# Kernel tuning notes

Hardware: AMD Instinct MI355X
Metric: run time of the kernel (lower is better)

The kernel has to match this reference:

```python
import jax, jax.numpy as jnp
import numpy as np

NS = 100000   # served nodes
NI = 100000   # interfered nodes
E = 1000000   # edges per relation
D = 64        # 2 * Nt_num, Nt_num = 32
HM = 32       # message MLP hidden
HU = 16       # update MLP hidden


def _lin_init(key, fan_in, fan_out):
    s = 1.0 / np.sqrt(fan_in)
    kw, kb = jax.random.split(key)
    w = jax.random.uniform(kw, (fan_in, fan_out), jnp.float32, -s, s)
    b = jax.random.uniform(kb, (fan_out,), jnp.float32, -s, s)
    return w, b


def setup_inputs() -> dict:
    key = jax.random.key(0)
    ks = jax.random.split(key, 12)
    wm1, bm1 = _lin_init(ks[0], D, HM)
    wm2, bm2 = _lin_init(ks[1], HM, D)
    wu1, bu1 = _lin_init(ks[2], D, HU)
    wu2, bu2 = _lin_init(ks[3], HU, D)
    wo, bo = _lin_init(ks[4], D, D)
    edge_s2i = jnp.stack([
        jax.random.randint(ks[5], (E,), 0, NS),   # src in served
        jax.random.randint(ks[6], (E,), 0, NI),   # dst in interfered
    ]).astype(jnp.int64)
    edge_i2s = jnp.stack([
        jax.random.randint(ks[7], (E,), 0, NI),   # src in interfered
        jax.random.randint(ks[8], (E,), 0, NS),   # dst in served
    ]).astype(jnp.int64)
    return {
        "x_served": jax.random.normal(ks[9], (NS, D), jnp.float32),
        "x_interfered": jax.random.normal(ks[10], (NI, D), jnp.float32),
        "edge_s2i": edge_s2i,
        "edge_i2s": edge_i2s,
        "wm1": wm1, "bm1": bm1, "wm2": wm2, "bm2": bm2,
        "wu1": wu1, "bu1": bu1, "wu2": wu2, "bu2": bu2,
        "wo": wo, "bo": bo,
    }


def reference(x_served, x_interfered, edge_s2i, edge_i2s,
              wm1, bm1, wm2, bm2, wu1, bu1, wu2, bu2, wo, bo):
    def mlp_m(h):  # MLP([D, 32, D]): Lin+ReLU, Lin+ReLU
        return jax.nn.relu(jax.nn.relu(h @ wm1 + bm1) @ wm2 + bm2)

    def mlp_u(h):  # MLP([D, 16, D])
        return jax.nn.relu(jax.nn.relu(h @ wu1 + bu1) @ wu2 + bu2)

    def conv(x_src, edges, n_dst):
        # gather source node features per edge, per-edge message MLP
        msg = mlp_m(x_src[edges[0]])                    # [E, D]
        # scatter-sum into destination nodes
        agg = jax.ops.segment_sum(msg, edges[1], num_segments=n_dst)
        return mlp_u(agg)                               # [n_dst, D]

    xs, xi = x_served, x_interfered
    for _ in range(3):
        new_i = conv(xs, edge_s2i, NI)   # served -> interfered
        new_s = conv(xi, edge_i2s, NS)   # interfered -> served
        xs, xi = new_s, new_i
    # h2o on served: Lin + Tanh -> beamforming matrix
    return jnp.tanh(xs @ wo + bo)
```

## Files before the change

kernel.cpp:

```cpp
#include <hip/hip_runtime.h>
#include <hip/hip_fp16.h>
#include <math.h>

constexpr int D = 64;
constexpr int CAP = 48;
constexpr int RPB = 256;
constexpr int EPB = 4096;

typedef _Float16 half2_t __attribute__((ext_vector_type(2)));
typedef _Float16 f16x8 __attribute__((ext_vector_type(8)));
typedef float f32x4 __attribute__((ext_vector_type(4)));

__device__ inline float fdot2(unsigned a, unsigned b, float c){
    return __builtin_amdgcn_fdot2(__builtin_bit_cast(half2_t, a),
                                  __builtin_bit_cast(half2_t, b), c, false);
}

__device__ inline unsigned pack2(float lo, float hi){
    __half2 h = __floats2half2_rn(lo, hi);
    return *(unsigned*)&h;
}

__device__ inline void ld16u(const unsigned* base, unsigned* w){
    const uint4* p = (const uint4*)base;
    uint4 a = p[0], b = p[1], c = p[2], d = p[3];
    w[0]=a.x;  w[1]=a.y;  w[2]=a.z;  w[3]=a.w;
    w[4]=b.x;  w[5]=b.y;  w[6]=b.z;  w[7]=b.w;
    w[8]=c.x;  w[9]=c.y;  w[10]=c.z; w[11]=c.w;
    w[12]=d.x; w[13]=d.y; w[14]=d.z; w[15]=d.w;
}

__device__ inline void store_half8(__half* dst, const float* o){
    uint4 w;
    w.x = pack2(o[0], o[1]); w.y = pack2(o[2], o[3]);
    w.z = pack2(o[4], o[5]); w.w = pack2(o[6], o[7]);
    *((uint4*)dst) = w;
}

__device__ inline void load_half8(const __half* src, float* r){
    uint4 w = *((const uint4*)src);
    __half2* h = (__half2*)&w;
    float2 f0 = __half22float2(h[0]);
    float2 f1 = __half22float2(h[1]);
    float2 f2 = __half22float2(h[2]);
    float2 f3 = __half22float2(h[3]);
    r[0] = f0.x; r[1] = f0.y; r[2] = f1.x; r[3] = f1.y;
    r[4] = f2.x; r[5] = f2.y; r[6] = f3.x; r[7] = f3.y;
}


__global__ void __launch_bounds__(256) k_bucket_mlpm(
        const int* __restrict__ es2i, const int* __restrict__ ei2s, int E, int NI,
        int NBUK, int BSTRIDE,
        int* __restrict__ gcur, unsigned* __restrict__ buckets,
        const float* __restrict__ x,
        const float* __restrict__ wm1, const float* __restrict__ bm1,
        const float* __restrict__ wm2, const float* __restrict__ bm2,
        __half* __restrict__ y, int Nmlp, int nbEdge)
{
    __shared__ __align__(16) char smem[8704];
    int t = threadIdx.x;

    if ((int)blockIdx.x < nbEdge){
        int* hist = (int*)smem;
        int* base = (int*)(smem + 4096);
        for (int i = t; i < NBUK; i += 256) hist[i] = 0;
        __syncthreads();
        int e0 = blockIdx.x * EPB + t;
        int rr[16], ss[16];
        #pragma unroll
        for (int k = 0; k < 16; k++){
            int i = e0 + k*256;
            if (i < E){
                ss[k] = es2i[i];            rr[k] = es2i[E + i];
            } else if (i < 2*E){
                int j = i - E;
                ss[k] = ei2s[j];            rr[k] = NI + ei2s[E + j];
            } else rr[k] = -1;
        }
        #pragma unroll
        for (int k = 0; k < 16; k++)
            if (rr[k] >= 0) atomicAdd(&hist[rr[k] >> 8], 1);
        __syncthreads();
        for (int b = t; b < NBUK; b += 256){
            int h = hist[b];
            base[b] = h ? atomicAdd(&gcur[b], h) : 0;
        }
        __syncthreads();
        #pragma unroll
        for (int k = 0; k < 16; k++){
            if (rr[k] >= 0){
                int b = rr[k] >> 8;
                int p = atomicAdd(&base[b], 1);
                if (p < BSTRIDE)
                    buckets[(size_t)b*BSTRIDE + p] =
                        ((unsigned)(rr[k] & 255) << 24) | (unsigned)ss[k];
            }
        }
        return;
    }

    unsigned* w1p = (unsigned*)smem;
    unsigned* w2p = (unsigned*)(smem + 4096);
    float*    sb1 = (float*)(smem + 8192);
    float*    sb2 = (float*)(smem + 8320);
    for (int i = t; i < 1024; i += 256){ int kp=i>>5, j=i&31; w1p[i]=pack2(wm1[(2*kp)*32+j], wm1[(2*kp+1)*32+j]); }
    for (int i = t; i < 1024; i += 256){ int jp=i>>6, c=i&63; w2p[i]=pack2(wm2[(2*jp)*64+c], wm2[(2*jp+1)*64+c]); }
    if (t < 32) sb1[t] = bm1[t];
    if (t < 64) sb2[t] = bm2[t];
    __syncthreads();
    int n = ((int)blockIdx.x - nbEdge)*256 + t;
    if (n >= Nmlp) return;

    const float4* xp = (const float4*)(x + (size_t)n*D);
    unsigned xq[32];
    #pragma unroll
    for (int i = 0; i < 16; i++){
        float4 v = xp[i];
        xq[2*i]   = pack2(v.x, v.y);
        xq[2*i+1] = pack2(v.z, v.w);
    }
    float h[32];
    #pragma unroll
    for (int j = 0; j < 32; j++) h[j] = 0.f;
    #pragma unroll
    for (int kp = 0; kp < 32; kp++){
        unsigned xv = xq[kp];
        unsigned w[32];
        ld16u(&w1p[kp*32],      w);
        ld16u(&w1p[kp*32 + 16], w + 16);
        #pragma unroll
        for (int j = 0; j < 32; j++) h[j] = fdot2(xv, w[j], h[j]);
    }
    #pragma unroll
    for (int j = 0; j < 32; j++) h[j] = fmaxf(h[j] + sb1[j], 0.f);
    unsigned hh[16];
    #pragma unroll
    for (int jp = 0; jp < 16; jp++) hh[jp] = pack2(h[2*jp], h[2*jp+1]);

    __half* yrow = y + (size_t)n*D;
    #pragma unroll
    for (int c0 = 0; c0 < 64; c0 += 32){
        float o[32];
        #pragma unroll
        for (int c = 0; c < 32; c++) o[c] = sb2[c0 + c];
        #pragma unroll
        for (int jp = 0; jp < 16; jp++){
            unsigned hv = hh[jp];
            unsigned w[32];
            ld16u(&w2p[jp*64 + c0],      w);
            ld16u(&w2p[jp*64 + c0 + 16], w + 16);
            #pragma unroll
            for (int c = 0; c < 32; c++) o[c] = fdot2(hv, w[c], o[c]);
        }
        #pragma unroll
        for (int c = 0; c < 32; c++) o[c] = fmaxf(o[c], 0.f);
        store_half8(yrow + c0,      &o[0]);
        store_half8(yrow + c0 + 8,  &o[8]);
        store_half8(yrow + c0 + 16, &o[16]);
        store_half8(yrow + c0 + 24, &o[24]);
    }
}


__global__ void __launch_bounds__(512) k_scatter_lds(const int* __restrict__ gcur,
        const unsigned* __restrict__ buckets, int BSTRIDE, int NTOT,
        int* __restrict__ cnt, int* __restrict__ slots)
{
    __shared__ int lcnt[RPB];
    __shared__ int lslots[RPB*CAP];
    int t = threadIdx.x;
    int b = blockIdx.x;
    int r0 = b * RPB;
    int nrows = NTOT - r0; if (nrows > RPB) nrows = RPB;

    for (int i = t; i < RPB; i += 512) lcnt[i] = 0;
    __syncthreads();

    int n = gcur[b]; if (n > BSTRIDE) n = BSTRIDE;
    const unsigned* bp = buckets + (size_t)b*BSTRIDE;
    for (int k = t; k < n; k += 512){
        unsigned e = bp[k];
        int lr  = e >> 24;
        int src = e & 0xFFFFFF;
        int pos = atomicAdd(&lcnt[lr], 1);
        if (pos < CAP) lslots[lr*CAP + pos] = src;
    }
    __syncthreads();

    int4* gs = (int4*)(slots + (size_t)r0*CAP);
    const int4* ls = (const int4*)lslots;
    int n4 = nrows*CAP/4;
    for (int i = t; i < n4; i += 512) gs[i] = ls[i];
    for (int i = t; i < nrows; i += 512) cnt[r0 + i] = lcnt[i];
}


__global__ void __launch_bounds__(256) k_agg(const __half* __restrict__ M,
        const int* __restrict__ cnt, const int* __restrict__ slots,
        __half* __restrict__ agg, int N)
{
    int gid  = blockIdx.x*256 + threadIdx.x;
    int node = gid >> 6;
    if (node >= N) return;
    int lane = gid & 63;
    int sub  = lane >> 3;
    int fl   = lane & 7;
    int deg = cnt[node]; deg = deg < CAP ? deg : CAP;
    const int* row = slots + (size_t)node*CAP;
    float acc[8];
    #pragma unroll
    for (int i = 0; i < 8; i++) acc[i] = 0.f;
    for (int k = sub; k < deg; k += 8){
        int s = row[k];
        float v[8];
        load_half8(M + (size_t)s*D + fl*8, v);
        #pragma unroll
        for (int i = 0; i < 8; i++) acc[i] += v[i];
    }
    #pragma unroll
    for (int i = 0; i < 8; i++){
        acc[i] += __shfl_xor(acc[i], 8);
        acc[i] += __shfl_xor(acc[i], 16);
        acc[i] += __shfl_xor(acc[i], 32);
    }
    if (sub == 0) store_half8(agg + (size_t)node*D + fl*8, acc);
}


__global__ void __launch_bounds__(256) k_mlp_um(const __half* __restrict__ agg,
        const float* __restrict__ wu1, const float* __restrict__ bu1,
        const float* __restrict__ wu2, const float* __restrict__ bu2,
        const float* __restrict__ wm1, const float* __restrict__ bm1,
        const float* __restrict__ wm2, const float* __restrict__ bm2,
        __half* __restrict__ y, int N)
{
    __shared__ float  lds_h [4][16][20];
    __shared__ float  lds_y [4][16][68];
    __shared__ float  lds_hm[4][16][36];
    __shared__ __half lds_m [4][16][72];

    int t  = threadIdx.x;
    int wv = t >> 6, l = t & 63;
    int m  = l & 15, g = l >> 4;

    f16x8 Bu1[2], Bu2[4], Bm1[2][2], Bm2[4];
    #pragma unroll
    for (int kt = 0; kt < 2; kt++)
        #pragma unroll
        for (int i = 0; i < 8; i++)
            Bu1[kt][i] = (_Float16)wu1[(kt*32 + 8*g + i)*16 + m];
    #pragma unroll
    for (int jb = 0; jb < 4; jb++)
        #pragma unroll
        for (int i = 0; i < 8; i++){
            int k = 8*g + i;
            Bu2[jb][i] = (k < 16) ? (_Float16)wu2[k*64 + jb*16 + m] : (_Float16)0.f;
        }
    #pragma unroll
    for (int kt = 0; kt < 2; kt++)
        #pragma unroll
        for (int nt = 0; nt < 2; nt++)
            #pragma unroll
            for (int i = 0; i < 8; i++)
                Bm1[kt][nt][i] = (_Float16)wm1[(kt*32 + 8*g + i)*32 + nt*16 + m];
    #pragma unroll
    for (int jb = 0; jb < 4; jb++)
        #pragma unroll
        for (int i = 0; i < 8; i++)
            Bm2[jb][i] = (_Float16)wm2[(8*g + i)*64 + jb*16 + m];

    float bu1v = bu1[m];
    float bu2v[4], bm2v[4], bm1v[2];
    #pragma unroll
    for (int jb = 0; jb < 4; jb++){ bu2v[jb] = bu2[jb*16 + m]; bm2v[jb] = bm2[jb*16 + m]; }
    #pragma unroll
    for (int nt = 0; nt < 2; nt++) bm1v[nt] = bm1[nt*16 + m];

    #pragma unroll
    for (int tile = 0; tile < 2; tile++){
        int nb = blockIdx.x*128 + tile*64 + wv*16;
        if (nb >= N) break;

        int an = nb + m; if (an >= N) an = N - 1;
        const __half* arow = agg + (size_t)an*64;
        f16x8 Ax0 = *reinterpret_cast<const f16x8*>(arow + 8*g);
        f16x8 Ax1 = *reinterpret_cast<const f16x8*>(arow + 32 + 8*g);

        f32x4 acc = {0.f, 0.f, 0.f, 0.f};
        acc = __builtin_amdgcn_mfma_f32_16x16x32_f16(Ax0, Bu1[0], acc, 0, 0, 0);
        acc = __builtin_amdgcn_mfma_f32_16x16x32_f16(Ax1, Bu1[1], acc, 0, 0, 0);
        #pragma unroll
        for (int r = 0; r < 4; r++)
            lds_h[wv][4*g + r][m] = fmaxf(acc[r] + bu1v, 0.f);

        f16x8 Ah;
        #pragma unroll
        for (int i = 0; i < 8; i++){
            int k = 8*g + i;
            Ah[i] = (k < 16) ? (_Float16)lds_h[wv][m][k] : (_Float16)0.f;
        }

        #pragma unroll
        for (int jb = 0; jb < 4; jb++){
            f32x4 a2 = {0.f, 0.f, 0.f, 0.f};
            a2 = __builtin_amdgcn_mfma_f32_16x16x32_f16(Ah, Bu2[jb], a2, 0, 0, 0);
            #pragma unroll
            for (int r = 0; r < 4; r++)
                lds_y[wv][4*g + r][jb*16 + m] = fmaxf(a2[r] + bu2v[jb], 0.f);
        }

        f16x8 Ay0, Ay1;
        #pragma unroll
        for (int i = 0; i < 8; i++){
            Ay0[i] = (_Float16)lds_y[wv][m][8*g + i];
            Ay1[i] = (_Float16)lds_y[wv][m][32 + 8*g + i];
        }

        #pragma unroll
        for (int nt = 0; nt < 2; nt++){
            f32x4 a3 = {0.f, 0.f, 0.f, 0.f};
            a3 = __builtin_amdgcn_mfma_f32_16x16x32_f16(Ay0, Bm1[0][nt], a3, 0, 0, 0);
            a3 = __builtin_amdgcn_mfma_f32_16x16x32_f16(Ay1, Bm1[1][nt], a3, 0, 0, 0);
            #pragma unroll
            for (int r = 0; r < 4; r++)
                lds_hm[wv][4*g + r][nt*16 + m] = fmaxf(a3[r] + bm1v[nt], 0.f);
        }

        f16x8 Ahm;
        #pragma unroll
        for (int i = 0; i < 8; i++)
            Ahm[i] = (_Float16)lds_hm[wv][m][8*g + i];

        #pragma unroll
        for (int jb = 0; jb < 4; jb++){
            f32x4 a4 = {0.f, 0.f, 0.f, 0.f};
            a4 = __builtin_amdgcn_mfma_f32_16x16x32_f16(Ahm, Bm2[jb], a4, 0, 0, 0);
            #pragma unroll
            for (int r = 0; r < 4; r++)
                lds_m[wv][4*g + r][jb*16 + m] = __float2half(fmaxf(a4[r] + bm2v[jb], 0.f));
        }

        int lr = l >> 2;
        int node = nb + lr;
        if (node < N){
            uint4* dst = (uint4*)(y + (size_t)node*64);
            const uint4* src = (const uint4*)&lds_m[wv][lr][0];
            int c = l & 3;
            dst[c]     = src[c];
            dst[c + 4] = src[c + 4];
        }
    }
}


__device__ inline float fast_tanh(float x){
    float ax = fabsf(x);
    float e  = __expf(2.f*ax);
    float t  = 1.f - 2.f/(e + 1.f);
    return copysignf(t, x);
}

__global__ void __launch_bounds__(256) k_mlp_uo(const __half* __restrict__ agg,
        const float* __restrict__ wu1, const float* __restrict__ bu1,
        const float* __restrict__ wu2, const float* __restrict__ bu2,
        const float* __restrict__ wo,  const float* __restrict__ bo,
        float* __restrict__ out, int N)
{
    __shared__ __align__(16) unsigned w1p[32*16];
    __shared__ __align__(16) unsigned w2p[8*64];
    __shared__ __align__(16) unsigned wop[32*64];
    __shared__ float sbu1[16], sbu2[64], sbo[64];
    __shared__ float stage[256*65];
    int t = threadIdx.x;
    for (int i = t; i < 512;  i += 256){ int kp=i>>4, j=i&15; w1p[i]=pack2(wu1[(2*kp)*16+j], wu1[(2*kp+1)*16+j]); }
    for (int i = t; i < 512;  i += 256){ int jp=i>>6, c=i&63; w2p[i]=pack2(wu2[(2*jp)*64+c], wu2[(2*jp+1)*64+c]); }
    for (int i = t; i < 2048; i += 256){ int kp=i>>6, c=i&63; wop[i]=pack2(wo[(2*kp)*64+c], wo[(2*kp+1)*64+c]); }
    if (t < 16) sbu1[t] = bu1[t];
    if (t < 64) sbu2[t] = bu2[t];
    if (t < 64) sbo[t]  = bo[t];
    __syncthreads();
    int n = blockIdx.x*256 + t;

    if (n < N){
        unsigned xq[32];
        {
            const uint4* p = (const uint4*)(agg + (size_t)n*D);
            #pragma unroll
            for (int i = 0; i < 8; i++){
                uint4 w = p[i];
                xq[4*i] = w.x; xq[4*i+1] = w.y; xq[4*i+2] = w.z; xq[4*i+3] = w.w;
            }
        }

        float h[16];
        #pragma unroll
        for (int j = 0; j < 16; j++) h[j] = 0.f;
        #pragma unroll
        for (int kp = 0; kp < 32; kp++){
            unsigned a = xq[kp];
            unsigned w[16];
            ld16u(&w1p[kp*16], w);
            #pragma unroll
            for (int j = 0; j < 16; j++) h[j] = fdot2(a, w[j], h[j]);
        }
        #pragma unroll
        for (int j = 0; j < 16; j++) h[j] = fmaxf(h[j] + sbu1[j], 0.f);
        unsigned hp[8];
        #pragma unroll
        for (int jp = 0; jp < 8; jp++) hp[jp] = pack2(h[2*jp], h[2*jp+1]);

        #pragma unroll
        for (int c0 = 0; c0 < 64; c0 += 32){
            float o[32];
            #pragma unroll
            for (int c = 0; c < 32; c++) o[c] = sbu2[c0 + c];
            #pragma unroll
            for (int jp = 0; jp < 8; jp++){
                unsigned a = hp[jp];
                unsigned w[32];
                ld16u(&w2p[jp*64 + c0],      w);
                ld16u(&w2p[jp*64 + c0 + 16], w + 16);
                #pragma unroll
                for (int c = 0; c < 32; c++) o[c] = fdot2(a, w[c], o[c]);
            }
            #pragma unroll
            for (int c = 0; c < 32; c += 2)
                xq[(c0 + c) >> 1] = pack2(fmaxf(o[c], 0.f), fmaxf(o[c+1], 0.f));
        }

        float* srow = &stage[t*65];
        #pragma unroll
        for (int c0 = 0; c0 < 64; c0 += 32){
            float o[32];
            #pragma unroll
            for (int c = 0; c < 32; c++) o[c] = sbo[c0 + c];
            #pragma unroll
            for (int kp = 0; kp < 32; kp++){
                unsigned a = xq[kp];
                unsigned w[32];
                ld16u(&wop[kp*64 + c0],      w);
                ld16u(&wop[kp*64 + c0 + 16], w + 16);
                #pragma unroll
                for (int c = 0; c < 32; c++) o[c] = fdot2(a, w[c], o[c]);
            }
            #pragma unroll
            for (int c = 0; c < 32; c++) srow[c0 + c] = fast_tanh(o[c]);
        }
    }
    __syncthreads();

    size_t blkbase = (size_t)blockIdx.x * 256 * 64;
    size_t limit   = (size_t)N * 64;
    #pragma unroll
    for (int k = 0; k < 16; k++){
        int f = k*256 + t;
        size_t e = blkbase + (size_t)f*4;
        if (e < limit){
            int ln = f >> 4;
            int c4 = (f & 15) * 4;
            float4 v;
            v.x = stage[ln*65 + c4];
            v.y = stage[ln*65 + c4 + 1];
            v.z = stage[ln*65 + c4 + 2];
            v.w = stage[ln*65 + c4 + 3];
            *((float4*)(out + e)) = v;
        }
    }
}


extern "C" void kernel_launch(void* const* d_in, const int* in_sizes, int n_in,
                              void* d_out, int out_size, void* d_ws, size_t ws_size,
                              hipStream_t stream)
{
    const float* x_interfered = (const float*)d_in[1];
    const int*   e_s2i        = (const int*)d_in[2];
    const int*   e_i2s        = (const int*)d_in[3];
    const float* wm1 = (const float*)d_in[4];  const float* bm1 = (const float*)d_in[5];
    const float* wm2 = (const float*)d_in[6];  const float* bm2 = (const float*)d_in[7];
    const float* wu1 = (const float*)d_in[8];  const float* bu1 = (const float*)d_in[9];
    const float* wu2 = (const float*)d_in[10]; const float* bu2 = (const float*)d_in[11];
    const float* wo  = (const float*)d_in[12]; const float* bo  = (const float*)d_in[13];

    const int NS = in_sizes[0] / D;
    const int NI = in_sizes[1] / D;
    const int E  = in_sizes[2] / 2;
    const int NMAX = (NS > NI) ? NS : NI;
    const int NTOT = NI + NS;

    const int NBUK = ((NTOT - 1) >> 8) + 1;
    int avg = (2*E) / NBUK;
    const int BSTRIDE = ((2*avg) + 1023) & ~1023;

    char* p = (char*)d_ws;
    auto alloc = [&](size_t bytes) -> void* {
        void* r = (void*)p;
        p += (bytes + 255) & ~(size_t)255;
        return r;
    };
    __half*   M      = (__half*)alloc((size_t)NMAX*D*2);
    __half*   AGG    = (__half*)alloc((size_t)NMAX*D*2);
    int*      cnt    = (int*)alloc((size_t)NTOT*4);
    int*      gcur   = (int*)alloc((size_t)NBUK*4);
    int*      slots  = (int*)alloc((size_t)NTOT*CAP*4);
    unsigned* buckets= (unsigned*)alloc((size_t)NBUK*BSTRIDE*4);
    (void)ws_size; (void)n_in; (void)out_size;

    const int* cnt_i = cnt;
    const int* cnt_s = cnt + NI;
    const int* slots_i = slots;
    const int* slots_s = slots + (size_t)NI*CAP;

    hipMemsetAsync(gcur, 0, (size_t)NBUK*4, stream);

    const int nbEdge = (2*E + EPB - 1)/EPB;
    const int nbMlp  = (NI + 255)/256;
    k_bucket_mlpm<<<nbEdge + nbMlp, 256, 0, stream>>>(
        e_s2i, e_i2s, E, NI, NBUK, BSTRIDE, gcur, buckets,
        x_interfered, wm1, bm1, wm2, bm2, M, NI, nbEdge);
    k_scatter_lds<<<NBUK, 512, 0, stream>>>(gcur, buckets, BSTRIDE, NTOT, cnt, slots);

    k_agg<<<((size_t)NS*64 + 255)/256, 256, 0, stream>>>(M, cnt_s, slots_s, AGG, NS);
    k_mlp_um<<<(NS + 127)/128, 256, 0, stream>>>(AGG, wu1, bu1, wu2, bu2,
                                               wm1, bm1, wm2, bm2, M, NS);
    k_agg<<<((size_t)NI*64 + 255)/256, 256, 0, stream>>>(M, cnt_i, slots_i, AGG, NI);
    k_mlp_um<<<(NI + 127)/128, 256, 0, stream>>>(AGG, wu1, bu1, wu2, bu2,
                                               wm1, bm1, wm2, bm2, M, NI);
    k_agg<<<((size_t)NS*64 + 255)/256, 256, 0, stream>>>(M, cnt_s, slots_s, AGG, NS);
    k_mlp_uo<<<(NS + 255)/256, 256, 0, stream>>>(AGG, wu1, bu1, wu2, bu2,
                                               wo, bo, (float*)d_out, NS);
}
```

Before: 232.6 us.

## Rewrite final update+output MLP kernel using 16x16x32 MFMA per wave

The final update-MLP plus output-linear-tanh kernel now computes each 16-node tile with MFMA f16 matrix instructions instead of per-thread fdot2 loops. Weights are held in registers as B fragments, and small per-wave LDS buffers move activations between layers. Each block handles 128 nodes in two tiles. The aim is to cut the ALU-bound dot-product work and the large 256x65 staging buffer, at the cost of per-thread scalar weight loads from global memory and some wasted zero-padded MFMA work for the 16-wide hidden layer.

```diff
diff --git a/kernel.cpp b/kernel.cpp
--- a/kernel.cpp
+++ b/kernel.cpp
@@ -367,104 +367,100 @@
         const float* __restrict__ wo,  const float* __restrict__ bo,
         float* __restrict__ out, int N)
 {
-    __shared__ __align__(16) unsigned w1p[32*16];
-    __shared__ __align__(16) unsigned w2p[8*64];
-    __shared__ __align__(16) unsigned wop[32*64];
-    __shared__ float sbu1[16], sbu2[64], sbo[64];
-    __shared__ float stage[256*65];
-    int t = threadIdx.x;
-    for (int i = t; i < 512;  i += 256){ int kp=i>>4, j=i&15; w1p[i]=pack2(wu1[(2*kp)*16+j], wu1[(2*kp+1)*16+j]); }
-    for (int i = t; i < 512;  i += 256){ int jp=i>>6, c=i&63; w2p[i]=pack2(wu2[(2*jp)*64+c], wu2[(2*jp+1)*64+c]); }
-    for (int i = t; i < 2048; i += 256){ int kp=i>>6, c=i&63; wop[i]=pack2(wo[(2*kp)*64+c], wo[(2*kp+1)*64+c]); }
-    if (t < 16) sbu1[t] = bu1[t];
-    if (t < 64) sbu2[t] = bu2[t];
-    if (t < 64) sbo[t]  = bo[t];
-    __syncthreads();
-    int n = blockIdx.x*256 + t;
-
-    if (n < N){
-        unsigned xq[32];
-        {
-            const uint4* p = (const uint4*)(agg + (size_t)n*D);
-            #pragma unroll
-            for (int i = 0; i < 8; i++){
-                uint4 w = p[i];
-                xq[4*i] = w.x; xq[4*i+1] = w.y; xq[4*i+2] = w.z; xq[4*i+3] = w.w;
-            }
-        }
-
-        float h[16];
-        #pragma unroll
-        for (int j = 0; j < 16; j++) h[j] = 0.f;
-        #pragma unroll
-        for (int kp = 0; kp < 32; kp++){
-            unsigned a = xq[kp];
-            unsigned w[16];
-            ld16u(&w1p[kp*16], w);
-            #pragma unroll
-            for (int j = 0; j < 16; j++) h[j] = fdot2(a, w[j], h[j]);
-        }
-        #pragma unroll
-        for (int j = 0; j < 16; j++) h[j] = fmaxf(h[j] + sbu1[j], 0.f);
-        unsigned hp[8];
-        #pragma unroll
-        for (int jp = 0; jp < 8; jp++) hp[jp] = pack2(h[2*jp], h[2*jp+1]);
-
-        #pragma unroll
-        for (int c0 = 0; c0 < 64; c0 += 32){
-            float o[32];
-            #pragma unroll
-            for (int c = 0; c < 32; c++) o[c] = sbu2[c0 + c];
-            #pragma unroll
-            for (int jp = 0; jp < 8; jp++){
-                unsigned a = hp[jp];
-                unsigned w[32];
-                ld16u(&w2p[jp*64 + c0],      w);
-                ld16u(&w2p[jp*64 + c0 + 16], w + 16);
-                #pragma unroll
-                for (int c = 0; c < 32; c++) o[c] = fdot2(a, w[c], o[c]);
-            }
-            #pragma unroll
-            for (int c = 0; c < 32; c += 2)
-                xq[(c0 + c) >> 1] = pack2(fmaxf(o[c], 0.f), fmaxf(o[c+1], 0.f));
-        }
-
-        float* srow = &stage[t*65];
-        #pragma unroll
-        for (int c0 = 0; c0 < 64; c0 += 32){
-            float o[32];
-            #pragma unroll
-            for (int c = 0; c < 32; c++) o[c] = sbo[c0 + c];
-            #pragma unroll
-            for (int kp = 0; kp < 32; kp++){
-                unsigned a = xq[kp];
-                unsigned w[32];
-                ld16u(&wop[kp*64 + c0],      w);
-                ld16u(&wop[kp*64 + c0 + 16], w + 16);
-                #pragma unroll
-                for (int c = 0; c < 32; c++) o[c] = fdot2(a, w[c], o[c]);
-            }
-            #pragma unroll
-            for (int c = 0; c < 32; c++) srow[c0 + c] = fast_tanh(o[c]);
-        }
-    }
-    __syncthreads();
-
-    size_t blkbase = (size_t)blockIdx.x * 256 * 64;
-    size_t limit   = (size_t)N * 64;
-    #pragma unroll
-    for (int k = 0; k < 16; k++){
-        int f = k*256 + t;
-        size_t e = blkbase + (size_t)f*4;
-        if (e < limit){
-            int ln = f >> 4;
-            int c4 = (f & 15) * 4;
-            float4 v;
-            v.x = stage[ln*65 + c4];
-            v.y = stage[ln*65 + c4 + 1];
-            v.z = stage[ln*65 + c4 + 2];
-            v.w = stage[ln*65 + c4 + 3];
-            *((float4*)(out + e)) = v;
+    __shared__ float lds_h[4][16][20];
+    __shared__ float lds_y[4][16][68];
+    __shared__ float lds_o[4][16][68];
+
+    int t  = threadIdx.x;
+    int wv = t >> 6, l = t & 63;
+    int m  = l & 15, g = l >> 4;
+
+    f16x8 Bu1[2], Bu2[4], Bo[2][4];
+    #pragma unroll
+    for (int kt = 0; kt < 2; kt++)
+        #pragma unroll
+        for (int i = 0; i < 8; i++)
+            Bu1[kt][i] = (_Float16)wu1[(kt*32 + 8*g + i)*16 + m];
+    #pragma unroll
+    for (int jb = 0; jb < 4; jb++)
+        #pragma unroll
+        for (int i = 0; i < 8; i++){
+            int k = 8*g + i;
+            Bu2[jb][i] = (k < 16) ? (_Float16)wu2[k*64 + jb*16 + m] : (_Float16)0.f;
+        }
+    #pragma unroll
+    for (int kt = 0; kt < 2; kt++)
+        #pragma unroll
+        for (int jb = 0; jb < 4; jb++)
+            #pragma unroll
+            for (int i = 0; i < 8; i++)
+                Bo[kt][jb][i] = (_Float16)wo[(kt*32 + 8*g + i)*64 + jb*16 + m];
+
+    float bu1v = bu1[m];
+    float bu2v[4], bov[4];
+    #pragma unroll
+    for (int jb = 0; jb < 4; jb++){ bu2v[jb] = bu2[jb*16 + m]; bov[jb] = bo[jb*16 + m]; }
+
+    #pragma unroll
+    for (int tile = 0; tile < 2; tile++){
+        int nb = blockIdx.x*128 + tile*64 + wv*16;
+        if (nb >= N) break;
+
+        int an = nb + m; if (an >= N) an = N - 1;
+        const __half* arow = agg + (size_t)an*64;
+        f16x8 Ax0 = *reinterpret_cast<const f16x8*>(arow + 8*g);
+        f16x8 Ax1 = *reinterpret_cast<const f16x8*>(arow + 32 + 8*g);
+
+        f32x4 acc = {0.f, 0.f, 0.f, 0.f};
+        acc = __builtin_amdgcn_mfma_f32_16x16x32_f16(Ax0, Bu1[0], acc, 0, 0, 0);
+        acc = __builtin_amdgcn_mfma_f32_16x16x32_f16(Ax1, Bu1[1], acc, 0, 0, 0);
+        #pragma unroll
+        for (int r = 0; r < 4; r++)
+            lds_h[wv][4*g + r][m] = fmaxf(acc[r] + bu1v, 0.f);
+
+        f16x8 Ah;
+        #pragma unroll
+        for (int i = 0; i < 8; i++){
+            int k = 8*g + i;
+            Ah[i] = (k < 16) ? (_Float16)lds_h[wv][m][k] : (_Float16)0.f;
+        }
+
+        #pragma unroll
+        for (int jb = 0; jb < 4; jb++){
+            f32x4 a2 = {0.f, 0.f, 0.f, 0.f};
+            a2 = __builtin_amdgcn_mfma_f32_16x16x32_f16(Ah, Bu2[jb], a2, 0, 0, 0);
+            #pragma unroll
+            for (int r = 0; r < 4; r++)
+                lds_y[wv][4*g + r][jb*16 + m] = fmaxf(a2[r] + bu2v[jb], 0.f);
+        }
+
+        f16x8 Ay0, Ay1;
+        #pragma unroll
+        for (int i = 0; i < 8; i++){
+            Ay0[i] = (_Float16)lds_y[wv][m][8*g + i];
+            Ay1[i] = (_Float16)lds_y[wv][m][32 + 8*g + i];
+        }
+
+        #pragma unroll
+        for (int jb = 0; jb < 4; jb++){
+            f32x4 a3 = {0.f, 0.f, 0.f, 0.f};
+            a3 = __builtin_amdgcn_mfma_f32_16x16x32_f16(Ay0, Bo[0][jb], a3, 0, 0, 0);
+            a3 = __builtin_amdgcn_mfma_f32_16x16x32_f16(Ay1, Bo[1][jb], a3, 0, 0, 0);
+            #pragma unroll
+            for (int r = 0; r < 4; r++)
+                lds_o[wv][4*g + r][jb*16 + m] = fast_tanh(a3[r] + bov[jb]);
+        }
+
+        int lr = l >> 2;
+        int node = nb + lr;
+        if (node < N){
+            float4* dst = (float4*)(out + (size_t)node*64);
+            const float4* src = (const float4*)&lds_o[wv][lr][0];
+            int c = l & 3;
+            dst[c]      = src[c];
+            dst[c + 4]  = src[c + 4];
+            dst[c + 8]  = src[c + 8];
+            dst[c + 12] = src[c + 12];
         }
     }
 }
@@ -528,6 +524,6 @@
     k_mlp_um<<<(NI + 127)/128, 256, 0, stream>>>(AGG, wu1, bu1, wu2, bu2,
                                                wm1, bm1, wm2, bm2, M, NI);
     k_agg<<<((size_t)NS*64 + 255)/256, 256, 0, stream>>>(M, cnt_s, slots_s, AGG, NS);
-    k_mlp_uo<<<(NS + 255)/256, 256, 0, stream>>>(AGG, wu1, bu1, wu2, bu2,
+    k_mlp_uo<<<(NS + 127)/128, 256, 0, stream>>>(AGG, wu1, bu1, wu2, bu2,
                                                wo, bo, (float*)d_out, NS);
 }
```

New measurement: 225.6 us. -3.0%, faster.
